# Optimization experiments

Hardware: AMD Instinct MI355X
Metric: run time of the kernel (lower is better)

Reference implementation:

```python
import jax, jax.numpy as jnp
import numpy as np

B, N, D, H = 256, 164, 1024, 8
NK = 100          # keypoint block size (hardcoded 100 in the module)
DH = D // H       # 128


def setup_inputs() -> dict:
    key = jax.random.key(0)
    ks = jax.random.split(key, 10)
    x = jax.random.normal(ks[0], (B, N, D), jnp.float32)
    xian = jax.random.normal(ks[1], (B, NK, NK), jnp.float32)
    # mask: True = masked. Keep the first NK columns unmasked so the dynamic-MLP
    # block never sees -finfo.max values (matches sane usage; avoids overflow).
    mask_tail = jax.random.bernoulli(ks[2], 0.1, (B, N - NK))
    mask = jnp.concatenate([jnp.zeros((B, NK), bool), mask_tail], axis=1)
    Wqkv = jax.random.normal(ks[3], (D, 3 * D), jnp.float32) * 0.02
    W1 = jax.random.normal(ks[4], (NK, 50), jnp.float32) * 0.1
    b1 = jnp.zeros((50,), jnp.float32)
    W2 = jax.random.normal(ks[5], (50, NK), jnp.float32) * 0.1
    b2 = jnp.zeros((NK,), jnp.float32)
    Wout = jax.random.normal(ks[6], (D, D), jnp.float32) * 0.02
    bout = jnp.zeros((D,), jnp.float32)
    return {"x": x, "mask": mask, "xian": xian, "Wqkv": Wqkv,
            "W1": W1, "b1": b1, "W2": W2, "b2": b2,
            "Wout": Wout, "bout": bout}


def reference(x, mask, xian, Wqkv, W1, b1, W2, b2, Wout, bout):
    scale = D ** -0.5  # scale_with_head=False -> dim**-0.5
    qkv = x @ Wqkv                                   # [B,N,3D]
    q, k, v = jnp.split(qkv, 3, axis=-1)
    def heads(t):
        return t.reshape(B, N, H, DH).transpose(0, 2, 1, 3)  # b h n d
    q, k, v = heads(q), heads(k), heads(v)
    dots = jnp.einsum('bhid,bhjd->bhij', q, k) * scale       # [B,H,N,N]
    mask_value = -jnp.finfo(dots.dtype).max
    dots = jnp.where(mask[:, None, None, :], mask_value, dots)
    # dynamic correction on the keypoint block
    aq = dots[:, :, :NK, :NK]                                # [B,H,100,100]
    lv = jax.nn.relu(jax.nn.relu(jax.nn.relu(aq) @ W1 + b1) @ W2 + b2)
    xin = aq + xian[:, None, :, :] * lv
    dots = dots.at[:, :, :NK, :NK].set(xin)
    attn = jax.nn.softmax(dots, axis=-1)
    out = jnp.einsum('bhij,bhjd->bhid', attn, v)             # [B,H,N,DH]
    out = out.transpose(0, 2, 1, 3).reshape(B, N, D)
    return out @ Wout + bout
```

## Files before the change

kernel.cpp:

```cpp
#include <hip/hip_runtime.h>
#include <hip/hip_bf16.h>
#include <cstdint>
#include <cstddef>

typedef __bf16 bf16;
typedef __attribute__((ext_vector_type(8))) __bf16 bf16x8;
typedef __attribute__((ext_vector_type(2))) __bf16 bf16x2;
typedef __attribute__((ext_vector_type(4))) __bf16 bf16x4;
typedef __attribute__((ext_vector_type(4))) float f32x4;

#define DEVI __device__ __forceinline__

constexpr int Bb = 256, Nn = 164, NKk = 100;
constexpr int Mm = Bb * Nn;
constexpr int JP = 192;

DEVI void gl_lds16(const void* g, void* l) {
  __builtin_amdgcn_global_load_lds(
      (const __attribute__((address_space(1))) void*)g,
      (__attribute__((address_space(3))) void*)l, 16, 0, 0);
}

DEVI int sw16(int row, int kb) { return row * 128 + ((kb ^ (row & 7)) * 8); }
DEVI int sw8(int row, int kb)  { return row * 64 + ((kb ^ (row & 7)) * 8); }

__global__ void k_cvt_bf16(const float* __restrict__ in, bf16* __restrict__ out, int n) {
  int stride = gridDim.x * blockDim.x;
  for (int i = blockIdx.x * blockDim.x + threadIdx.x; i < (n >> 2); i += stride) {
    float4 v = ((const float4*)in)[i];
    bf16x4 o;
    o[0] = (bf16)v.x; o[1] = (bf16)v.y; o[2] = (bf16)v.z; o[3] = (bf16)v.w;
    ((bf16x4*)out)[i] = o;
  }
}

__global__ void k_maskdet(const unsigned char* __restrict__ m, int* __restrict__ mode) {
  __shared__ int sbyte, sodd;
  if (threadIdx.x == 0) { sbyte = 0; sodd = 0; }
  __syncthreads();
  for (int i = threadIdx.x; i < Mm; i += 256)
    if ((i & 3) && m[i]) sbyte = 1;
  __syncthreads();
  if (sbyte == 0) {
    const int* m32 = (const int*)m;
    for (int i = 1 + 2 * (int)threadIdx.x; i < Mm; i += 512)
      if (m32[i] != 0) sodd = 1;
  }
  __syncthreads();
  if (threadIdx.x == 0) *mode = sbyte ? 1 : (sodd ? 0 : 2);
}

__global__ void k_prep_w(const float* __restrict__ W1, const float* __restrict__ W2,
                         bf16* __restrict__ w1t, bf16* __restrict__ w2t) {
  int tid = threadIdx.x;
  int4 z = make_int4(0, 0, 0, 0);
  for (int i = tid; i < 1024; i += 256) ((int4*)w1t)[i] = z;
  for (int i = tid; i < 896;  i += 256) ((int4*)w2t)[i] = z;
  __syncthreads();
  for (int idx = tid; idx < 5000; idx += 256) {
    int k = idx / 50, c = idx % 50;
    w1t[sw16(c, k >> 3) + (k & 7)] = (bf16)W1[idx];
  }
  for (int idx = tid; idx < 5000; idx += 256) {
    int c = idx / 100, jp = idx % 100;
    w2t[sw8(jp, c >> 3) + (c & 7)] = (bf16)W2[idx];
  }
}

__global__ void k_maskbias(const void* __restrict__ maskp, const int* __restrict__ mode,
                           float* __restrict__ mb) {
  int b = blockIdx.x, col = threadIdx.x;
  int mmode = *mode;
  float v;
  if (col < NKk) v = 0.f;
  else if (col < 164) {
    int mi = b * 164 + col;
    long long m = (mmode == 1) ? (long long)((const unsigned char*)maskp)[mi]
                : (mmode == 0) ? (long long)((const int*)maskp)[mi]
                               : ((const long long*)maskp)[mi];
    v = m ? -__FLT_MAX__ : 0.f;
  } else v = -__FLT_MAX__;
  mb[b * 192 + col] = v;
}

__global__ void k_xianT(const float* __restrict__ xian, float* __restrict__ xT) {
  __shared__ float t[32][33];
  int b = blockIdx.y;
  int gt = blockIdx.x & 3, jt = blockIdx.x >> 2;
  int tx = threadIdx.x & 31, ty = threadIdx.x >> 5;
#pragma unroll
  for (int i = 0; i < 4; ++i) {
    int gi = gt * 32 + ty + i * 8, jp = jt * 32 + tx;
    t[ty + i * 8][tx] = (gi < 100 && jp < 100) ? xian[((size_t)b * 100 + gi) * 100 + jp] : 0.f;
  }
  __syncthreads();
#pragma unroll
  for (int i = 0; i < 4; ++i) {
    int jp = jt * 32 + ty + i * 8, gi = gt * 32 + tx;
    if (jp < 100 && gi < 112)
      xT[((size_t)b * 100 + jp) * 112 + gi] = t[tx][ty + i * 8];
  }
}

__global__ void k_transpose_cvt(const float* __restrict__ in, bf16* __restrict__ out,
                                int R, int C) {
  __shared__ float tile[32][33];
  int c0 = blockIdx.x * 32, r0 = blockIdx.y * 32;
  int tx = threadIdx.x & 31, ty = threadIdx.x >> 5;
#pragma unroll
  for (int i = 0; i < 4; ++i) {
    int r = ty + i * 8;
    tile[r][tx] = in[(size_t)(r0 + r) * C + c0 + tx];
  }
  __syncthreads();
#pragma unroll
  for (int i = 0; i < 4; ++i) {
    int rr = ty + i * 8;
    out[(size_t)(c0 + rr) * R + r0 + tx] = (bf16)tile[tx][rr];
  }
}

template <int MODE>
__global__ __launch_bounds__(256) void k_gemm(const bf16* __restrict__ A,
                                              const bf16* __restrict__ Bt,
                                              void* __restrict__ Cout,
                                              const float* __restrict__ bias,
                                              bf16* __restrict__ vTout) {
  constexpr int K = 1024;
  constexpr int CLD = (MODE == 0) ? 3072 : 1024;
  __shared__ bf16 As[128 * 32];
  __shared__ bf16 Bs[128 * 32];
  constexpr int ETSZ = (MODE == 0) ? 128 * 136 : 1;
  __shared__ bf16 Et[ETSZ];
  const int tid = threadIdx.x, lane = tid & 63, w = tid >> 6;
  const int l15 = lane & 15, l4 = lane >> 4;
  const int wm = w >> 1, wn = w & 1;

  const int lin = blockIdx.y * gridDim.x + blockIdx.x;
  const int cpx = (gridDim.x * gridDim.y) >> 3;
  const int swz = (lin & 7) * cpx + (lin >> 3);
  const int tileM = (swz / gridDim.x) * 128, tileN = (swz % gridDim.x) * 128;

  f32x4 acc[4][4];
#pragma unroll
  for (int mi = 0; mi < 4; ++mi)
#pragma unroll
    for (int ni = 0; ni < 4; ++ni) acc[mi][ni] = f32x4{0.f, 0.f, 0.f, 0.f};

  for (int k0 = 0; k0 < K; k0 += 32) {
    __syncthreads();
#pragma unroll
    for (int i = 0; i < 2; ++i) {
      int c = w * 2 + i;
      int blk = c * 64 + lane;
      int r = blk >> 2, sl = blk & 3;
      int kb = sl ^ ((r >> 1) & 3);
      gl_lds16(A + (size_t)(tileM + r) * K + k0 + kb * 8, (char*)As + c * 1024);
      gl_lds16(Bt + (size_t)(tileN + r) * K + k0 + kb * 8, (char*)Bs + c * 1024);
    }
    __syncthreads();
    bf16x8 af[4], bfr[4];
#pragma unroll
    for (int mi = 0; mi < 4; ++mi) {
      int r = wm * 64 + mi * 16 + l15;
      af[mi] = *(const bf16x8*)&As[r * 32 + ((l4 ^ ((r >> 1) & 3)) * 8)];
    }
#pragma unroll
    for (int ni = 0; ni < 4; ++ni) {
      int r = wn * 64 + ni * 16 + l15;
      bfr[ni] = *(const bf16x8*)&Bs[r * 32 + ((l4 ^ ((r >> 1) & 3)) * 8)];
    }
#pragma unroll
    for (int mi = 0; mi < 4; ++mi)
#pragma unroll
      for (int ni = 0; ni < 4; ++ni)
        acc[mi][ni] = __builtin_amdgcn_mfma_f32_16x16x32_bf16(af[mi], bfr[ni], acc[mi][ni], 0, 0, 0);
  }

  if (MODE == 0 && tileN >= 2048) {
    const int h = (tileN - 2048) >> 7;
#pragma unroll
    for (int mi = 0; mi < 4; ++mi)
#pragma unroll
      for (int ni = 0; ni < 4; ++ni) {
        int nr = wn * 64 + ni * 16 + l15;
        int mr = wm * 64 + mi * 16 + l4 * 4;
        bf16x4 pv;
#pragma unroll
        for (int j = 0; j < 4; ++j) pv[j] = (bf16)acc[mi][ni][j];
        *(bf16x4*)&Et[nr * 136 + mr] = pv;
      }
    __syncthreads();
#pragma unroll
    for (int it = 0; it < 32; ++it) {
      int dh = w * 32 + it;
#pragma unroll
      for (int hf = 0; hf < 2; ++hf) {
        int mrel = hf * 64 + lane;
        int m = tileM + mrel;
        int b = m / 164, j = m - b * 164;
        vTout[((size_t)(b * 8 + h) * 128 + dh) * JP + j] = Et[dh * 136 + mrel];
      }
    }
  } else {
#pragma unroll
    for (int mi = 0; mi < 4; ++mi)
#pragma unroll
      for (int ni = 0; ni < 4; ++ni)
#pragma unroll
        for (int j = 0; j < 4; ++j) {
          int m = tileM + wm * 64 + mi * 16 + l4 * 4 + j;
          int n = tileN + wn * 64 + ni * 16 + l15;
          float v = acc[mi][ni][j];
          if (MODE == 0)
            ((bf16*)Cout)[(size_t)m * CLD + n] = (bf16)v;
          else
            ((float*)Cout)[(size_t)m * CLD + n] = v + bias[n];
        }
  }
}

__global__ __launch_bounds__(704, 3) void k_attn(
    const bf16* __restrict__ qkv, const bf16* __restrict__ vT,
    const bf16* __restrict__ w1t_g, const bf16* __restrict__ w2t_g,
    const float* __restrict__ maskbias, const float* __restrict__ xianT,
    const float* __restrict__ b1, const float* __restrict__ b2,
    bf16* __restrict__ aout) {
  __shared__ __align__(16) char smem[160448];
  bf16* VTs = (bf16*)smem;
  bf16* Ks  = (bf16*)(smem + 49152);
  bf16* AQs = (bf16*)(smem + 49152);
  bf16* Pw0 = (bf16*)(smem + 94208);
  bf16* W1T = (bf16*)(smem + 128000);
  bf16* H1s = (bf16*)(smem + 128000);
  bf16* W2T = (bf16*)(smem + 144384);
  float* biasL = (float*)(smem + 158720);
  float* b1L = (float*)(smem + 159744);
  float* b2L = (float*)(smem + 160000);

  const int tid = threadIdx.x, lane = tid & 63, w = tid >> 6;
  const int l15 = lane & 15, l4 = lane >> 4;
  const int i0 = blockIdx.x;
  const int bh = (i0 & 7) * 256 + (i0 >> 3);
  const int b = bh >> 3, h = bh & 7;
  const int rq = w * 16;
  const int pr12 = l15 % 12;

  bf16x8 qf[4];
  {
    int qrow = rq + l15; if (qrow > 163) qrow = 163;
    const bf16* qbase = qkv + (size_t)(b * 164 + qrow) * 3072 + h * 128;
#pragma unroll
    for (int kk = 0; kk < 4; ++kk)
      qf[kk] = *(const bf16x8*)(qbase + kk * 32 + l4 * 8);
  }

  for (int c = w; c < 41; c += 11) {
    int blk = c * 64 + lane;
    int r = blk >> 4, sl = blk & 15;
    int kb = sl ^ (r & 7);
    gl_lds16(qkv + (size_t)(b * 164 + r) * 3072 + 1024 + h * 128 + kb * 8, (char*)Ks + c * 1024);
  }
  for (int c = w; c < 48; c += 11) {
    int blk = c * 64 + lane;
    int dh = blk / 24, sl = blk % 24;
    int kb = sl - (dh % 24); if (kb < 0) kb += 24;
    gl_lds16(vT + ((size_t)bh * 128 + dh) * JP + kb * 8, (char*)VTs + c * 1024);
  }
  for (int c = w; c < 16; c += 11)
    gl_lds16(w1t_g + c * 512 + lane * 8, (char*)W1T + c * 1024);
  for (int c = w; c < 14; c += 11)
    gl_lds16(w2t_g + c * 512 + lane * 8, (char*)W2T + c * 1024);
  if (w == 10 && lane < 48)
    gl_lds16(maskbias + b * 192 + lane * 4, (char*)biasL);
  if (tid < 192) {
    int r = 164 + (tid >> 4), sl = tid & 15;
    ((int4*)Ks)[r * 16 + sl] = make_int4(0, 0, 0, 0);
  }
  if (tid < 64) b1L[tid] = (tid < 50) ? b1[tid] : 0.f;
  else if (tid < 176) { int c = tid - 64; b2L[c] = (c < 100) ? b2[c] : 0.f; }
  __syncthreads();

  constexpr float SC = 0.03125f;
  f32x4 s[11];
#pragma unroll
  for (int nt = 0; nt < 11; ++nt) {
    f32x4 acc = f32x4{0.f, 0.f, 0.f, 0.f};
#pragma unroll
    for (int kk = 0; kk < 4; ++kk) {
      bf16x8 kf = *(const bf16x8*)&Ks[sw16(nt * 16 + l15, kk * 4 + l4)];
      acc = __builtin_amdgcn_mfma_f32_16x16x32_bf16(kf, qf[kk], acc, 0, 0, 0);
    }
    f32x4 bv = *(const f32x4*)&biasL[nt * 16 + l4 * 4];
#pragma unroll
    for (int j = 0; j < 4; ++j) acc[j] = acc[j] * SC + bv[j];
    s[nt] = acc;
  }
  __syncthreads();

  if (w < 7) {
    int q = rq + l15;
#pragma unroll
    for (int nt = 0; nt < 8; ++nt) {
#pragma unroll
      for (int pr = 0; pr < 2; ++pr) {
        int k0 = nt * 16 + l4 * 4 + pr * 2;
        float v0 = (q < 100 && k0 < 100)     ? fmaxf(s[nt][pr * 2], 0.f)     : 0.f;
        float v1 = (q < 100 && k0 + 1 < 100) ? fmaxf(s[nt][pr * 2 + 1], 0.f) : 0.f;
        bf16x2 pv; pv[0] = (bf16)v0; pv[1] = (bf16)v1;
        *(bf16x2*)&AQs[sw16(q, k0 >> 3) + (k0 & 7)] = pv;
      }
    }
  }
  __syncthreads();

  f32x4 a1[3];
#pragma unroll
  for (int it = 0; it < 3; ++it) {
    int t = w + it * 11;
    f32x4 acc = f32x4{0.f, 0.f, 0.f, 0.f};
    if (t < 28) {
      int qs = t >> 2, ct = t & 3;
#pragma unroll
      for (int kk = 0; kk < 4; ++kk) {
        bf16x8 wf = *(const bf16x8*)&W1T[sw16(ct * 16 + l15, kk * 4 + l4)];
        bf16x8 af = *(const bf16x8*)&AQs[sw16(qs * 16 + l15, kk * 4 + l4)];
        acc = __builtin_amdgcn_mfma_f32_16x16x32_bf16(wf, af, acc, 0, 0, 0);
      }
    }
    a1[it] = acc;
  }
  __syncthreads();
#pragma unroll
  for (int it = 0; it < 3; ++it) {
    int t = w + it * 11;
    if (t < 28) {
      int qs = t >> 2, ct = t & 3;
      int qrow = qs * 16 + l15;
#pragma unroll
      for (int pr = 0; pr < 2; ++pr) {
        int c0 = ct * 16 + l4 * 4 + pr * 2;
        float v0 = (c0 < 50)     ? fmaxf(a1[it][pr * 2] + b1L[c0], 0.f)         : 0.f;
        float v1 = (c0 + 1 < 50) ? fmaxf(a1[it][pr * 2 + 1] + b1L[c0 + 1], 0.f) : 0.f;
        bf16x2 pv; pv[0] = (bf16)v0; pv[1] = (bf16)v1;
        *(bf16x2*)&H1s[sw8(qrow, c0 >> 3) + (c0 & 7)] = pv;
      }
    }
  }
  __syncthreads();

  if (w < 7) {
    int q = rq + l15;
#pragma unroll
    for (int nt2 = 0; nt2 < 7; ++nt2) {
      f32x4 acc = f32x4{0.f, 0.f, 0.f, 0.f};
#pragma unroll
      for (int kk = 0; kk < 2; ++kk) {
        bf16x8 wf = *(const bf16x8*)&W2T[sw8(nt2 * 16 + l15, kk * 4 + l4)];
        bf16x8 hf = *(const bf16x8*)&H1s[sw8(rq + l15, kk * 4 + l4)];
        acc = __builtin_amdgcn_mfma_f32_16x16x32_bf16(wf, hf, acc, 0, 0, 0);
      }
#pragma unroll
      for (int j = 0; j < 4; ++j) {
        int jp = nt2 * 16 + l4 * 4 + j;
        if (jp < 100 && q < 100) {
          float lv = fmaxf(acc[j] + b2L[jp], 0.f);
          s[nt2][j] += xianT[((size_t)b * 100 + jp) * 112 + q] * lv;
        }
      }
    }
  }

  float mx = -__FLT_MAX__;
#pragma unroll
  for (int nt = 0; nt < 11; ++nt)
#pragma unroll
    for (int j = 0; j < 4; ++j) mx = fmaxf(mx, s[nt][j]);
  mx = fmaxf(mx, __shfl_xor(mx, 16));
  mx = fmaxf(mx, __shfl_xor(mx, 32));
  float sum = 0.f;
#pragma unroll
  for (int nt = 0; nt < 11; ++nt)
#pragma unroll
    for (int j = 0; j < 4; ++j) { float e = __expf(s[nt][j] - mx); s[nt][j] = e; sum += e; }
  sum += __shfl_xor(sum, 16);
  sum += __shfl_xor(sum, 32);
  float rinv = 1.f / sum;

  bf16x2 pp[11][2];
#pragma unroll
  for (int nt = 0; nt < 11; ++nt)
#pragma unroll
    for (int pr = 0; pr < 2; ++pr) {
      bf16x2 pv;
      pv[0] = (bf16)(s[nt][pr * 2] * rinv);
      pv[1] = (bf16)(s[nt][pr * 2 + 1] * rinv);
      pp[nt][pr] = pv;
    }

  bf16* PwB = Pw0 + w * 1536;
  f32x4 o[8];
#pragma unroll
  for (int i = 0; i < 8; ++i) o[i] = f32x4{0.f, 0.f, 0.f, 0.f};
  int vmr[8];
#pragma unroll
  for (int i = 0; i < 8; ++i) vmr[i] = (i * 16 + l15) % 24;
#pragma unroll
  for (int hh = 0; hh < 2; ++hh) {
#pragma unroll
    for (int nn = 0; nn < 6; ++nn) {
      int nt = hh * 6 + nn;
      if (nt < 11) {
        int slot = nn * 2 + (l4 >> 1);
        int rs = slot + pr12; if (rs >= 12) rs -= 12;
#pragma unroll
        for (int pr = 0; pr < 2; ++pr)
          *(bf16x2*)&PwB[l15 * 96 + rs * 8 + (l4 & 1) * 4 + pr * 2] = pp[nt][pr];
      }
    }
#pragma unroll
    for (int kk2 = 0; kk2 < 3; ++kk2) {
      int rs = kk2 * 4 + l4 + pr12; if (rs >= 12) rs -= 12;
      bf16x8 af = *(const bf16x8*)&PwB[l15 * 96 + rs * 8];
#pragma unroll
      for (int i = 0; i < 8; ++i) {
        int sb = 12 * hh + kk2 * 4 + l4 + vmr[i]; if (sb >= 24) sb -= 24;
        bf16x8 bb = *(const bf16x8*)&VTs[(i * 16 + l15) * 192 + sb * 8];
        o[i] = __builtin_amdgcn_mfma_f32_16x16x32_bf16(af, bb, o[i], 0, 0, 0);
      }
    }
  }

#pragma unroll
  for (int i = 0; i < 8; ++i) {
    int dh = i * 16 + l15;
#pragma unroll
    for (int j = 0; j < 4; ++j) {
      int q = rq + l4 * 4 + j;
      if (q < 164)
        aout[(size_t)(b * 164 + q) * 1024 + h * 128 + dh] = (bf16)o[i][j];
    }
  }
}

extern "C" void kernel_launch(void* const* d_in, const int* in_sizes, int n_in,
                              void* d_out, int out_size, void* d_ws, size_t ws_size,
                              hipStream_t stream) {
  const float* x    = (const float*)d_in[0];
  const void* mask  = (const void*)d_in[1];
  const float* xian = (const float*)d_in[2];
  const float* Wqkv = (const float*)d_in[3];
  const float* W1   = (const float*)d_in[4];
  const float* b1   = (const float*)d_in[5];
  const float* W2   = (const float*)d_in[6];
  const float* b2   = (const float*)d_in[7];
  const float* Wout = (const float*)d_in[8];
  const float* bout = (const float*)d_in[9];
  float* out = (float*)d_out;
  char* ws = (char*)d_ws;

  bf16* xb    = (bf16*)(ws);
  bf16* wqkvT = (bf16*)(ws + 85983232ULL);
  bf16* woutT = (bf16*)(ws + 92274688ULL);
  bf16* qkvb  = (bf16*)(ws + 94371840ULL);
  bf16* vTb   = (bf16*)(ws + 352321536ULL);
  bf16* aoutb = (bf16*)(ws + 452984832ULL);
  int*   mmode    = (int*)(ws + 1024);
  bf16*  w1t_g    = (bf16*)(ws + 4096);
  bf16*  w2t_g    = (bf16*)(ws + 20480);
  float* maskbias = (float*)(ws + 36864);
  float* xianTp   = (float*)(ws + 262144);

  k_cvt_bf16<<<2048, 256, 0, stream>>>(x, xb, Mm * 1024);
  k_transpose_cvt<<<dim3(96, 32), 256, 0, stream>>>(Wqkv, wqkvT, 1024, 3072);
  k_transpose_cvt<<<dim3(32, 32), 256, 0, stream>>>(Wout, woutT, 1024, 1024);
  k_gemm<0><<<dim3(24, 328), 256, 0, stream>>>(xb, wqkvT, (void*)qkvb, nullptr, vTb);
  k_maskdet<<<1, 256, 0, stream>>>((const unsigned char*)mask, mmode);
  k_prep_w<<<1, 256, 0, stream>>>(W1, W2, w1t_g, w2t_g);
  k_maskbias<<<256, 192, 0, stream>>>(mask, mmode, maskbias);
  k_xianT<<<dim3(16, 256), 256, 0, stream>>>(xian, xianTp);
  k_attn<<<2048, 704, 0, stream>>>(qkvb, vTb, w1t_g, w2t_g, maskbias, xianTp,
                                   b1, b2, aoutb);
  k_gemm<1><<<dim3(8, 328), 256, 0, stream>>>(aoutb, woutT, (void*)out, bout, nullptr);
}
```

Measured before the change: 852.2 us.

## Enlarge GEMM tiles to 256x256 with double-buffered LDS prefetch

Rewrites both projection GEMMs to use 256x256 output tiles, 512 threads and a K-step of 64. Global-to-LDS loads for the next K-step are issued during the current step's MFMAs through a double buffer, with MFMA priority raised. The V-transpose epilogue now writes vectorized bf16 chunks. The goal is more data reuse per tile and hiding load latency. In exchange it uses 128KB of LDS per block and many more registers, which limits occupancy, and the tile count (1968) leaves a partial wave.

```diff
diff --git a/kernel.cpp b/kernel.cpp
--- a/kernel.cpp
+++ b/kernel.cpp
@@ -23,6 +23,17 @@
 
 DEVI int sw16(int row, int kb) { return row * 128 + ((kb ^ (row & 7)) * 8); }
 DEVI int sw8(int row, int kb)  { return row * 64 + ((kb ^ (row & 7)) * 8); }
+
+DEVI void barrier_raw() {
+  asm volatile("" ::: "memory");
+  __builtin_amdgcn_s_barrier();
+  asm volatile("" ::: "memory");
+}
+DEVI void vm0_barrier() {
+  asm volatile("s_waitcnt vmcnt(0)" ::: "memory");
+  __builtin_amdgcn_s_barrier();
+  asm volatile("" ::: "memory");
+}
 
 __global__ void k_cvt_bf16(const float* __restrict__ in, bf16* __restrict__ out, int n) {
   int stride = gridDim.x * blockDim.x;
@@ -121,102 +132,161 @@
 }
 
 template <int MODE>
-__global__ __launch_bounds__(256) void k_gemm(const bf16* __restrict__ A,
-                                              const bf16* __restrict__ Bt,
-                                              void* __restrict__ Cout,
-                                              const float* __restrict__ bias,
-                                              bf16* __restrict__ vTout) {
+__global__ __launch_bounds__(512, 2) void k_gemm(const bf16* __restrict__ A,
+                                                 const bf16* __restrict__ Bt,
+                                                 void* __restrict__ Cout,
+                                                 const float* __restrict__ bias,
+                                                 bf16* __restrict__ vTout) {
   constexpr int K = 1024;
-  constexpr int CLD = (MODE == 0) ? 3072 : 1024;
-  __shared__ bf16 As[128 * 32];
-  __shared__ bf16 Bs[128 * 32];
-  constexpr int ETSZ = (MODE == 0) ? 128 * 136 : 1;
-  __shared__ bf16 Et[ETSZ];
+  constexpr int NT = 16;
+  __shared__ __align__(16) char smem[131072];
+
   const int tid = threadIdx.x, lane = tid & 63, w = tid >> 6;
   const int l15 = lane & 15, l4 = lane >> 4;
-  const int wm = w >> 1, wn = w & 1;
-
-  const int lin = blockIdx.y * gridDim.x + blockIdx.x;
-  const int cpx = (gridDim.x * gridDim.y) >> 3;
+  const int wm = w >> 2, wn = w & 3;
+
+  const int nbx = (MODE == 0) ? 12 : 4;
+  const int lin = blockIdx.x;
+  const int cpx = gridDim.x >> 3;
   const int swz = (lin & 7) * cpx + (lin >> 3);
-  const int tileM = (swz / gridDim.x) * 128, tileN = (swz % gridDim.x) * 128;
-
-  f32x4 acc[4][4];
-#pragma unroll
-  for (int mi = 0; mi < 4; ++mi)
-#pragma unroll
-    for (int ni = 0; ni < 4; ++ni) acc[mi][ni] = f32x4{0.f, 0.f, 0.f, 0.f};
-
-  for (int k0 = 0; k0 < K; k0 += 32) {
-    __syncthreads();
-#pragma unroll
-    for (int i = 0; i < 2; ++i) {
-      int c = w * 2 + i;
-      int blk = c * 64 + lane;
-      int r = blk >> 2, sl = blk & 3;
-      int kb = sl ^ ((r >> 1) & 3);
-      gl_lds16(A + (size_t)(tileM + r) * K + k0 + kb * 8, (char*)As + c * 1024);
-      gl_lds16(Bt + (size_t)(tileN + r) * K + k0 + kb * 8, (char*)Bs + c * 1024);
-    }
-    __syncthreads();
-    bf16x8 af[4], bfr[4];
-#pragma unroll
-    for (int mi = 0; mi < 4; ++mi) {
-      int r = wm * 64 + mi * 16 + l15;
-      af[mi] = *(const bf16x8*)&As[r * 32 + ((l4 ^ ((r >> 1) & 3)) * 8)];
-    }
-#pragma unroll
-    for (int ni = 0; ni < 4; ++ni) {
-      int r = wn * 64 + ni * 16 + l15;
-      bfr[ni] = *(const bf16x8*)&Bs[r * 32 + ((l4 ^ ((r >> 1) & 3)) * 8)];
-    }
-#pragma unroll
-    for (int mi = 0; mi < 4; ++mi)
-#pragma unroll
-      for (int ni = 0; ni < 4; ++ni)
-        acc[mi][ni] = __builtin_amdgcn_mfma_f32_16x16x32_bf16(af[mi], bfr[ni], acc[mi][ni], 0, 0, 0);
+  const int tileM = (swz / nbx) * 256, tileN = (swz % nbx) * 256;
+
+  size_t aoff[4], boff[4]; int loff[4];
+#pragma unroll
+  for (int li = 0; li < 4; ++li) {
+    int idx = li * 512 + tid;
+    int row = idx >> 3, sl = idx & 7;
+    int kb = sl ^ (row & 7);
+    aoff[li] = (size_t)(tileM + row) * K + kb * 8;
+    boff[li] = (size_t)(tileN + row) * K + kb * 8;
+    loff[li] = idx * 16;
+  }
+
+  f32x4 acc[8][4];
+#pragma unroll
+  for (int mf = 0; mf < 8; ++mf)
+#pragma unroll
+    for (int nf = 0; nf < 4; ++nf) acc[mf][nf] = f32x4{0.f, 0.f, 0.f, 0.f};
+
+#pragma unroll
+  for (int li = 0; li < 4; ++li) {
+    gl_lds16(A + aoff[li], smem + loff[li]);
+    gl_lds16(Bt + boff[li], smem + 65536 + loff[li]);
+  }
+
+  for (int t = 0; t < NT; ++t) {
+    const int coff = (t & 1) << 15;
+    const char* Ac = smem + coff;
+    const char* Bc = smem + 65536 + coff;
+    char* An = smem + (coff ^ 32768);
+    char* Bn = smem + 65536 + (coff ^ 32768);
+    const int kadd = (t + 1) * 64;
+    const bool st = (t + 1) < NT;
+
+    vm0_barrier();
+
+    bf16x8 bfr[4][2];
+#pragma unroll
+    for (int nf = 0; nf < 4; ++nf) {
+      int row = wn * 64 + nf * 16 + l15;
+#pragma unroll
+      for (int kk = 0; kk < 2; ++kk)
+        bfr[nf][kk] = *(const bf16x8*)(Bc + row * 128 + (((kk * 4 + l4) ^ (row & 7)) * 16));
+    }
+
+#pragma unroll
+    for (int ph = 0; ph < 4; ++ph) {
+      if (st) {
+#pragma unroll
+        for (int q = 0; q < 2; ++q) {
+          int li = (ph & 1) * 2 + q;
+          if (ph < 2) gl_lds16(A + aoff[li] + kadd, An + loff[li]);
+          else        gl_lds16(Bt + boff[li] + kadd, Bn + loff[li]);
+        }
+      }
+      bf16x8 af[2][2];
+#pragma unroll
+      for (int mi = 0; mi < 2; ++mi) {
+        int row = wm * 128 + (ph * 2 + mi) * 16 + l15;
+#pragma unroll
+        for (int kk = 0; kk < 2; ++kk)
+          af[mi][kk] = *(const bf16x8*)(Ac + row * 128 + (((kk * 4 + l4) ^ (row & 7)) * 16));
+      }
+      __builtin_amdgcn_s_setprio(1);
+#pragma unroll
+      for (int mi = 0; mi < 2; ++mi)
+#pragma unroll
+        for (int nf = 0; nf < 4; ++nf)
+#pragma unroll
+          for (int kk = 0; kk < 2; ++kk)
+            acc[ph * 2 + mi][nf] = __builtin_amdgcn_mfma_f32_16x16x32_bf16(
+                af[mi][kk], bfr[nf][kk], acc[ph * 2 + mi][nf], 0, 0, 0);
+      __builtin_amdgcn_s_setprio(0);
+      barrier_raw();
+    }
   }
 
   if (MODE == 0 && tileN >= 2048) {
-    const int h = (tileN - 2048) >> 7;
-#pragma unroll
-    for (int mi = 0; mi < 4; ++mi)
-#pragma unroll
-      for (int ni = 0; ni < 4; ++ni) {
-        int nr = wn * 64 + ni * 16 + l15;
-        int mr = wm * 64 + mi * 16 + l4 * 4;
-        bf16x4 pv;
-#pragma unroll
-        for (int j = 0; j < 4; ++j) pv[j] = (bf16)acc[mi][ni][j];
-        *(bf16x4*)&Et[nr * 136 + mr] = pv;
-      }
-    __syncthreads();
-#pragma unroll
-    for (int it = 0; it < 32; ++it) {
-      int dh = w * 32 + it;
-#pragma unroll
-      for (int hf = 0; hf < 2; ++hf) {
-        int mrel = hf * 64 + lane;
-        int m = tileM + mrel;
+    const int h0 = (tileN - 2048) >> 7;
+    bf16* Et = (bf16*)smem;
+#pragma unroll
+    for (int nh = 0; nh < 2; ++nh) {
+      barrier_raw();
+      if ((wn >> 1) == nh) {
+#pragma unroll
+        for (int mf = 0; mf < 8; ++mf)
+#pragma unroll
+          for (int nf = 0; nf < 4; ++nf) {
+            int nr = (wn & 1) * 64 + nf * 16 + l15;
+            int mr = wm * 128 + mf * 16 + l4 * 4;
+            bf16x4 pv;
+#pragma unroll
+            for (int j = 0; j < 4; ++j) pv[j] = (bf16)acc[mf][nf][j];
+            *(bf16x4*)&Et[nr * 264 + mr] = pv;
+          }
+      }
+      barrier_raw();
+#pragma unroll
+      for (int r8 = 0; r8 < 8; ++r8) {
+        int idx = r8 * 512 + tid;
+        int nr = idx >> 5, m8 = (idx & 31) * 8;
+        bf16x8 v = *(const bf16x8*)&Et[nr * 264 + m8];
+        int m = tileM + m8;
         int b = m / 164, j = m - b * 164;
-        vTout[((size_t)(b * 8 + h) * 128 + dh) * JP + j] = Et[dh * 136 + mrel];
+        if (j + 7 < 164) {
+          size_t base = ((size_t)(b * 8 + h0 + nh) * 128 + nr) * JP + j;
+          bf16x4 lo, hi;
+#pragma unroll
+          for (int e = 0; e < 4; ++e) { lo[e] = v[e]; hi[e] = v[e + 4]; }
+          *(bf16x4*)&vTout[base] = lo;
+          *(bf16x4*)&vTout[base + 4] = hi;
+        } else {
+#pragma unroll
+          for (int e = 0; e < 8; ++e) {
+            int me = m + e; int be = me / 164, je = me - be * 164;
+            vTout[((size_t)(be * 8 + h0 + nh) * 128 + nr) * JP + je] = v[e];
+          }
+        }
       }
     }
   } else {
 #pragma unroll
-    for (int mi = 0; mi < 4; ++mi)
-#pragma unroll
-      for (int ni = 0; ni < 4; ++ni)
-#pragma unroll
-        for (int j = 0; j < 4; ++j) {
-          int m = tileM + wm * 64 + mi * 16 + l4 * 4 + j;
-          int n = tileN + wn * 64 + ni * 16 + l15;
-          float v = acc[mi][ni][j];
-          if (MODE == 0)
-            ((bf16*)Cout)[(size_t)m * CLD + n] = (bf16)v;
-          else
-            ((float*)Cout)[(size_t)m * CLD + n] = v + bias[n];
+    for (int mf = 0; mf < 8; ++mf)
+#pragma unroll
+      for (int nf = 0; nf < 4; ++nf) {
+        int m0 = tileM + wm * 128 + mf * 16 + l4 * 4;
+        int n = tileN + wn * 64 + nf * 16 + l15;
+        if (MODE == 0) {
+#pragma unroll
+          for (int j = 0; j < 4; ++j)
+            ((bf16*)Cout)[(size_t)(m0 + j) * 3072 + n] = (bf16)acc[mf][nf][j];
+        } else {
+          float bv = bias[n];
+#pragma unroll
+          for (int j = 0; j < 4; ++j)
+            ((float*)Cout)[(size_t)(m0 + j) * 1024 + n] = acc[mf][nf][j] + bv;
         }
+      }
   }
 }
 
@@ -474,12 +544,12 @@
   k_cvt_bf16<<<2048, 256, 0, stream>>>(x, xb, Mm * 1024);
   k_transpose_cvt<<<dim3(96, 32), 256, 0, stream>>>(Wqkv, wqkvT, 1024, 3072);
   k_transpose_cvt<<<dim3(32, 32), 256, 0, stream>>>(Wout, woutT, 1024, 1024);
-  k_gemm<0><<<dim3(24, 328), 256, 0, stream>>>(xb, wqkvT, (void*)qkvb, nullptr, vTb);
+  k_gemm<0><<<1968, 512, 0, stream>>>(xb, wqkvT, (void*)qkvb, nullptr, vTb);
   k_maskdet<<<1, 256, 0, stream>>>((const unsigned char*)mask, mmode);
   k_prep_w<<<1, 256, 0, stream>>>(W1, W2, w1t_g, w2t_g);
   k_maskbias<<<256, 192, 0, stream>>>(mask, mmode, maskbias);
   k_xianT<<<dim3(16, 256), 256, 0, stream>>>(xian, xianTp);
   k_attn<<<2048, 704, 0, stream>>>(qkvb, vTb, w1t_g, w2t_g, maskbias, xianTp,
                                    b1, b2, aoutb);
-  k_gemm<1><<<dim3(8, 328), 256, 0, stream>>>(aoutb, woutT, (void*)out, bout, nullptr);
-}
+  k_gemm<1><<<656, 512, 0, stream>>>(aoutb, woutT, (void*)out, bout, nullptr);
+}
```

Result: faster. 752.1 us (-11.7%).
